# Optimization experiments

Measured on AMD Instinct MI355X. Metric: run time of the kernel, lower is better.

The kernel has to match this reference:

```python
import jax, jax.numpy as jnp
import numpy as np

N_CELLS, IN_DIM, HID, OUT = 65536, 128, 256, 128
MLP_H = 128   # engine MLP hidden width is hard-coded to 128 in the source
N_MORPH = 32  # min(32, n_cells//4)


def setup_inputs() -> dict:
    key = jax.random.key(0)
    ks = jax.random.split(key, 18)
    s = 0.05
    return {
        "x": jax.random.normal(ks[0], (1, IN_DIM), jnp.float32),
        "hiddens": jax.random.normal(ks[1], (N_CELLS, HID), jnp.float32) * 0.1,
        "Wa1": jax.random.normal(ks[2], (MLP_H, IN_DIM + HID), jnp.float32) * s,
        "ba1": jax.random.normal(ks[3], (MLP_H,), jnp.float32) * s,
        "Wa2": jax.random.normal(ks[4], (OUT, MLP_H), jnp.float32) * s,
        "ba2": jax.random.normal(ks[5], (OUT,), jnp.float32) * s,
        "Wg1": jax.random.normal(ks[6], (MLP_H, IN_DIM + HID), jnp.float32) * s,
        "bg1": jax.random.normal(ks[7], (MLP_H,), jnp.float32) * s,
        "Wg2": jax.random.normal(ks[8], (OUT, MLP_H), jnp.float32) * s,
        "bg2": jax.random.normal(ks[9], (OUT,), jnp.float32) * s,
        "W_ih": jax.random.normal(ks[10], (3 * HID, OUT + 1), jnp.float32) * s,
        "W_hh": jax.random.normal(ks[11], (3 * HID, HID), jnp.float32) * s,
        "b_ih": jax.random.normal(ks[12], (3 * HID,), jnp.float32) * s,
        "b_hh": jax.random.normal(ks[13], (3 * HID,), jnp.float32) * s,
        "nat_w": jnp.eye(HID, dtype=jnp.float32),  # nn.init.eye_
        "morph_w": jax.random.normal(ks[14], (N_MORPH, HID, HID), jnp.float32) * 0.02,
        "morph_src": jax.random.randint(ks[15], (N_MORPH,), 0, N_CELLS, jnp.int32),
        "morph_tgt": jax.random.randint(ks[16], (N_MORPH,), 0, N_CELLS, jnp.int32),
        "step": 0,
    }


def _forward(x, hiddens, Wa1, ba1, Wa2, ba2, Wg1, bg1, Wg2, bg2,
             W_ih, W_hh, b_ih, b_hh, nat_w, morph_w, morph_src, morph_tgt, step):
    n = hiddens.shape[0]
    # --- BenchMind, batched over all cells (x broadcast to every cell) ---
    xb = jnp.broadcast_to(x, (n, x.shape[-1]))
    combined = jnp.concatenate([xb, hiddens], axis=-1)               # [n, in+hid]
    a = jax.nn.relu(combined @ Wa1.T + ba1) @ Wa2.T + ba2            # [n, out]
    g = jax.nn.relu(combined @ Wg1.T + bg1) @ Wg2.T + bg2            # [n, out]
    out = a - g                                                       # [n, out]
    tension = jnp.mean(out * out, axis=-1, keepdims=True)            # [n, 1]
    # mem_input is detached in torch
    mem_in = jax.lax.stop_gradient(jnp.concatenate([out, tension], axis=-1))
    # --- PyTorch GRUCell math ---
    gi = mem_in @ W_ih.T + b_ih                                      # [n, 3H]
    gh = hiddens @ W_hh.T + b_hh                                     # [n, 3H]
    i_r, i_z, i_n = jnp.split(gi, 3, axis=-1)
    h_r, h_z, h_n = jnp.split(gh, 3, axis=-1)
    r = jax.nn.sigmoid(i_r + h_r)
    z = jax.nn.sigmoid(i_z + h_z)
    nn_ = jnp.tanh(i_n + r * h_n)
    hid = jax.lax.stop_gradient((1.0 - z) * nn_ + z * hiddens)       # detached new hiddens
    if step % 3 == 0:
        hid = jax.lax.stop_gradient(hid @ nat_w.T)                   # natural transformation
    # --- limit / colimit (morphism gather-transform-aggregate) ---
    limit = jnp.einsum('mij,mj->i', morph_w, hid[morph_src]) / N_MORPH
    colimit = jnp.einsum('mji,mj->i', morph_w, hid[morph_tgt]) / N_MORPH
    diff = limit - colimit
    cat_tension = jnp.mean(diff * diff)
    hid = hid + 0.05 * jax.lax.stop_gradient(diff)[None, :]
    # --- faction sync (+ debate if step > 5) ---
    n_f = min(8, n // 2)
    fs = n // n_f
    hf = hid[: n_f * fs].reshape(n_f, fs, hid.shape[-1])
    fmean = hf.mean(axis=1, keepdims=True)                           # [n_f,1,H]
    hf = 0.85 * hf + 0.15 * fmean
    if step > 5:
        global_op = hf.mean(axis=1).mean(axis=0)                     # mean of faction means
        dc = max(1, fs // 4)
        hf = hf.at[:, :dc].set(0.85 * hf[:, :dc] + 0.15 * global_op)
    hid = jnp.concatenate([hf.reshape(n_f * fs, -1), hid[n_f * fs:]], axis=0)
    # --- tension-weighted combination (weights detached: .item() in torch) ---
    t = jax.lax.stop_gradient(tension[:, 0])                         # [n]
    w = jax.nn.softmax(t, axis=0)
    combined_out = jnp.sum(w[:, None] * out, axis=0, keepdims=True)  # [1, out]
    avg_tension = jnp.mean(tension) + 0.1 * cat_tension
    return combined_out, avg_tension, hid


def reference(x, hiddens, Wa1, ba1, Wa2, ba2, Wg1, bg1, Wg2, bg2,
              W_ih, W_hh, b_ih, b_hh, nat_w, morph_w, morph_src, morph_tgt, step):
    combined_out, avg_tension, _ = _forward(
        x, hiddens, Wa1, ba1, Wa2, ba2, Wg1, bg1, Wg2, bg2,
        W_ih, W_hh, b_ih, b_hh, nat_w, morph_w, morph_src, morph_tgt, step)
    return combined_out, avg_tension
```

## Files before the change

kernel.cpp:

```cpp
#include <hip/hip_runtime.h>
#include <math.h>

#define OFF_W1B   0
#define OFF_W2A   32768
#define OFF_XW1B  49152
#define OFF_B2D   49408
#define OFF_PT    49536
#define OFF_PE    50560
#define OFF_POUT  51584
#define OFF_MI4   182656
#define OFF_TEN   190848
#define OFF_HH4   190912
#define OFF_GI    207296
#define OFF_GH    256448
#define OFF_PLIM  305600
#define OFF_PCOL8 313792
#define OFF_GMSK  379392

typedef short bf16x8 __attribute__((ext_vector_type(8)));
typedef short s16x4  __attribute__((ext_vector_type(4)));
typedef float f32x4  __attribute__((ext_vector_type(4)));

__device__ __forceinline__ unsigned short f2bf(float f) {
    unsigned u = __builtin_bit_cast(unsigned, f);
    u += 0x7FFFu + ((u >> 16) & 1u);
    return (unsigned short)(u >> 16);
}

__device__ __forceinline__ bf16x8 cvt8(float4 a, float4 b) {
    bf16x8 v;
    v[0] = (short)f2bf(a.x); v[1] = (short)f2bf(a.y);
    v[2] = (short)f2bf(a.z); v[3] = (short)f2bf(a.w);
    v[4] = (short)f2bf(b.x); v[5] = (short)f2bf(b.y);
    v[6] = (short)f2bf(b.z); v[7] = (short)f2bf(b.w);
    return v;
}

__global__ __launch_bounds__(256) void k_prep(
    const float* __restrict__ x, const float* __restrict__ hiddens,
    const float* __restrict__ Wa1, const float* __restrict__ ba1,
    const float* __restrict__ Wa2, const float* __restrict__ ba2,
    const float* __restrict__ Wg1, const float* __restrict__ bg1,
    const float* __restrict__ Wg2, const float* __restrict__ bg2,
    const int* __restrict__ msrc, const int* __restrict__ mtgt,
    float* __restrict__ ws)
{
    const int b = blockIdx.x, t = threadIdx.x;
    unsigned short* w1b = (unsigned short*)(ws + OFF_W1B);
    unsigned short* w2a = (unsigned short*)(ws + OFF_W2A);
    if (b < 256) {
        const int n = b;
        const float* row = (n < 128) ? &Wa1[n * 384] : &Wg1[(n - 128) * 384];
        const int kc = t >> 3;
        w1b[(kc * 256 + n) * 8 + (t & 7)] = f2bf(row[128 + t]);
        if (n < 128) {
            float w2 = (t < 128) ? Wa2[n * 128 + t] : -Wg2[n * 128 + (t - 128)];
            w2a[(kc * 128 + n) * 8 + (t & 7)] = f2bf(w2);
        }
    } else if (b == 256) {
        const int n = t;
        const float* wr = (n < 128) ? &Wa1[n * 384] : &Wg1[(n - 128) * 384];
        float s = (n < 128) ? ba1[n] : bg1[n - 128];
        for (int j = 0; j < 128; ++j) s = fmaf(x[j], wr[j], s);
        ws[OFF_XW1B + n] = s;
        if (n < 128) ws[OFF_B2D + n] = ba2[n] - bg2[n];
    } else if (b == 257) {
        unsigned long long* gm = (unsigned long long*)(ws + OFF_GMSK);
        for (int i = t; i < 1024; i += 256) gm[i] = 0ull;
        __syncthreads();
        if (t < 64) {
            const int cell = (t < 32) ? msrc[t] : mtgt[t - 32];
            atomicOr(&gm[cell >> 6], 1ull << t);
        }
    } else {
        const int g = b - 258;
        const int cell = (g < 32) ? msrc[g] : mtgt[g - 32];
        ws[OFF_HH4 + (t >> 2) * 256 + g * 4 + (t & 3)] = hiddens[(size_t)cell * 256 + t];
    }
}

__global__ __launch_bounds__(512, 2) void k_main(
    const float* __restrict__ hiddens,
    const int* __restrict__ msrc, const int* __restrict__ mtgt,
    float* __restrict__ ws)
{
    __shared__ __align__(16) short hB[64 * 256];
    __shared__ __align__(16) short h1B[64 * 256];
    __shared__ float part[512];
    __shared__ float e_sm[64], t_sm_[64];
    __shared__ int gid_sm[64];

    const int tid  = threadIdx.x;
    const int lane = tid & 63, wid = tid >> 6;
    const int l15 = lane & 15, l4 = lane >> 4;
    const int blk = blockIdx.x;

    if (tid < 64) gid_sm[tid] = (tid < 32) ? msrc[tid] : mtgt[tid - 32];

    const uint4* w1g = (const uint4*)(ws + OFF_W1B);
    const uint4* w2g = (const uint4*)(ws + OFF_W2A);
    const unsigned long long* gm = (const unsigned long long*)(ws + OFF_GMSK);

    const int rc = tid >> 3;
    const int q0 = (tid & 7) * 4;
    const float* hsrc = hiddens + (size_t)(blk * 128 + rc) * 256 + q0 * 8;

    float4 nx0, nx1, nx2, nx3, nx4, nx5, nx6, nx7;
    nx0 = *(const float4*)(hsrc + 0);  nx1 = *(const float4*)(hsrc + 4);
    nx2 = *(const float4*)(hsrc + 8);  nx3 = *(const float4*)(hsrc + 12);
    nx4 = *(const float4*)(hsrc + 16); nx5 = *(const float4*)(hsrc + 20);
    nx6 = *(const float4*)(hsrc + 24); nx7 = *(const float4*)(hsrc + 28);

    uint4 af[8][2], a2[8];
#pragma unroll
    for (int s = 0; s < 8; ++s) {
        af[s][0] = w1g[(s * 4 + l4) * 256 + wid * 32 + l15];
        af[s][1] = w1g[(s * 4 + l4) * 256 + wid * 32 + 16 + l15];
        a2[s]    = w2g[(s * 4 + l4) * 128 + wid * 16 + l15];
    }

    *(bf16x8*)&hB[rc * 256 + (((q0 + 0) ^ (rc & 15)) << 3)] = cvt8(nx0, nx1);
    *(bf16x8*)&hB[rc * 256 + (((q0 + 1) ^ (rc & 15)) << 3)] = cvt8(nx2, nx3);
    *(bf16x8*)&hB[rc * 256 + (((q0 + 2) ^ (rc & 15)) << 3)] = cvt8(nx4, nx5);
    *(bf16x8*)&hB[rc * 256 + (((q0 + 3) ^ (rc & 15)) << 3)] = cvt8(nx6, nx7);
    nx0 = *(const float4*)(hsrc + 16384 + 0);  nx1 = *(const float4*)(hsrc + 16384 + 4);
    nx2 = *(const float4*)(hsrc + 16384 + 8);  nx3 = *(const float4*)(hsrc + 16384 + 12);
    nx4 = *(const float4*)(hsrc + 16384 + 16); nx5 = *(const float4*)(hsrc + 16384 + 20);
    nx6 = *(const float4*)(hsrc + 16384 + 24); nx7 = *(const float4*)(hsrc + 16384 + 28);
    __syncthreads();

#pragma unroll
    for (int t = 0; t < 2; ++t) {
        const int bt = blk * 2 + t;

        f32x4 acc[2][4];
#pragma unroll
        for (int nf = 0; nf < 2; ++nf)
#pragma unroll
            for (int ct = 0; ct < 4; ++ct) acc[nf][ct] = (f32x4)0.f;

        __builtin_amdgcn_s_setprio(1);
#pragma unroll
        for (int s = 0; s < 8; ++s) {
            bf16x8 b[4];
#pragma unroll
            for (int ct = 0; ct < 4; ++ct) {
                const int c = ct * 16 + l15;
                b[ct] = *(const bf16x8*)&hB[c * 256 + (((s * 4 + l4) ^ (c & 15)) << 3)];
            }
#pragma unroll
            for (int nf = 0; nf < 2; ++nf) {
                const bf16x8 a = __builtin_bit_cast(bf16x8, af[s][nf]);
#pragma unroll
                for (int ct = 0; ct < 4; ++ct)
                    acc[nf][ct] = __builtin_amdgcn_mfma_f32_16x16x32_bf16(a, b[ct], acc[nf][ct], 0, 0, 0);
            }
        }
        __builtin_amdgcn_s_setprio(0);

#pragma unroll
        for (int nf = 0; nf < 2; ++nf) {
            const int n0 = wid * 32 + nf * 16 + l4 * 4;
            float4 xb = *(const float4*)(ws + OFF_XW1B + n0);
            const float bx[4] = {xb.x, xb.y, xb.z, xb.w};
            const int chunk = n0 >> 3;
            const int off = (l4 & 1) * 4;
#pragma unroll
            for (int ct = 0; ct < 4; ++ct) {
                const int c = ct * 16 + l15;
                s16x4 pk;
#pragma unroll
                for (int r = 0; r < 4; ++r)
                    pk[r] = (short)f2bf(fmaxf(acc[nf][ct][r] + bx[r], 0.f));
                *(s16x4*)&h1B[c * 256 + ((chunk ^ (c & 15)) << 3) + off] = pk;
            }
        }
        __syncthreads();

        f32x4 acc2[4];
#pragma unroll
        for (int ct = 0; ct < 4; ++ct) acc2[ct] = (f32x4)0.f;

        __builtin_amdgcn_s_setprio(1);
#pragma unroll
        for (int s = 0; s < 8; ++s) {
            bf16x8 b2[4];
#pragma unroll
            for (int ct = 0; ct < 4; ++ct) {
                const int c = ct * 16 + l15;
                b2[ct] = *(const bf16x8*)&h1B[c * 256 + (((s * 4 + l4) ^ (c & 15)) << 3)];
            }
            const bf16x8 a = __builtin_bit_cast(bf16x8, a2[s]);
#pragma unroll
            for (int ct = 0; ct < 4; ++ct)
                acc2[ct] = __builtin_amdgcn_mfma_f32_16x16x32_bf16(a, b2[ct], acc2[ct], 0, 0, 0);
        }
        __builtin_amdgcn_s_setprio(0);

        float outv[4][4];
        {
            float4 bd = *(const float4*)(ws + OFF_B2D + wid * 16 + l4 * 4);
            const float bv[4] = {bd.x, bd.y, bd.z, bd.w};
#pragma unroll
            for (int ct = 0; ct < 4; ++ct)
#pragma unroll
                for (int r = 0; r < 4; ++r)
                    outv[ct][r] = acc2[ct][r] + bv[r];
        }

#pragma unroll
        for (int ct = 0; ct < 4; ++ct) {
            float sq = 0.f;
#pragma unroll
            for (int r = 0; r < 4; ++r) sq = fmaf(outv[ct][r], outv[ct][r], sq);
            sq += __shfl_xor(sq, 16);
            sq += __shfl_xor(sq, 32);
            if (l4 == 0) part[wid * 64 + ct * 16 + l15] = sq;
        }
        __syncthreads();

        if (tid < 64) {
            float s = 0.f;
#pragma unroll
            for (int w = 0; w < 8; ++w) s += part[w * 64 + tid];
            const float tv = s * (1.f / 128.f);
            const float ev = expf(tv);
            t_sm_[tid] = tv; e_sm[tid] = ev;
            float pt = tv, pe = ev;
            for (int off = 32; off > 0; off >>= 1) {
                pt += __shfl_down(pt, off);
                pe += __shfl_down(pe, off);
            }
            if (tid == 0) { ws[OFF_PT + bt] = pt; ws[OFF_PE + bt] = pe; }
            unsigned long long m = gm[bt];
            while (m) {
                const int g = __builtin_ctzll(m); m &= m - 1;
                const int cg = gid_sm[g];
                if ((cg >> 6) == bt && (cg & 63) == tid) ws[OFF_TEN + g] = tv;
            }
        }
        __syncthreads();

        {
            float p[4];
#pragma unroll
            for (int r = 0; r < 4; ++r) {
                float s = 0.f;
#pragma unroll
                for (int ct = 0; ct < 4; ++ct)
                    s = fmaf(e_sm[ct * 16 + l15], outv[ct][r], s);
                p[r] = s;
            }
#pragma unroll
            for (int r = 0; r < 4; ++r) {
                p[r] += __shfl_xor(p[r], 1);
                p[r] += __shfl_xor(p[r], 2);
                p[r] += __shfl_xor(p[r], 4);
                p[r] += __shfl_xor(p[r], 8);
            }
            if (l15 == 0)
                *(float4*)(ws + OFF_POUT + (size_t)bt * 128 + wid * 16 + l4 * 4) =
                    make_float4(p[0], p[1], p[2], p[3]);
        }
        {
            unsigned long long m = gm[bt];
            while (m) {
                const int g = __builtin_ctzll(m); m &= m - 1;
                const int cg = gid_sm[g];
                if ((cg >> 6) != bt) continue;
                const int c = cg & 63;
                if ((c & 15) == l15) {
                    const int ct = c >> 4;
                    *(float4*)(ws + OFF_MI4 + (wid * 4 + l4) * 256 + g * 4) =
                        make_float4(outv[ct][0], outv[ct][1], outv[ct][2], outv[ct][3]);
                }
            }
        }

        if (t == 0) {
            *(bf16x8*)&hB[rc * 256 + (((q0 + 0) ^ (rc & 15)) << 3)] = cvt8(nx0, nx1);
            *(bf16x8*)&hB[rc * 256 + (((q0 + 1) ^ (rc & 15)) << 3)] = cvt8(nx2, nx3);
            *(bf16x8*)&hB[rc * 256 + (((q0 + 2) ^ (rc & 15)) << 3)] = cvt8(nx4, nx5);
            *(bf16x8*)&hB[rc * 256 + (((q0 + 3) ^ (rc & 15)) << 3)] = cvt8(nx6, nx7);
            __syncthreads();
        }
    }
}

__global__ __launch_bounds__(256) void k_tail1(
    const float* __restrict__ W_ih, const float* __restrict__ W_hh,
    const float* __restrict__ b_ih, const float* __restrict__ b_hh,
    float* __restrict__ ws)
{
    const int lane = threadIdx.x & 63;
    const int w    = threadIdx.x >> 6;
    const int row  = __builtin_amdgcn_readfirstlane(blockIdx.x * 4 + w);
    const float* mi4 = ws + OFF_MI4;
    const float* hh4 = ws + OFF_HH4;

    const float* wi = W_ih + row * 129;
    float gi = b_ih[row];
#pragma unroll 8
    for (int q = 0; q < 32; ++q) {
        float4 a = *(const float4*)(mi4 + q * 256 + lane * 4);
        gi = fmaf(wi[4 * q + 0], a.x, gi);
        gi = fmaf(wi[4 * q + 1], a.y, gi);
        gi = fmaf(wi[4 * q + 2], a.z, gi);
        gi = fmaf(wi[4 * q + 3], a.w, gi);
    }
    gi = fmaf(ws[OFF_TEN + lane], wi[128], gi);

    const float* wh = W_hh + (size_t)row * 256;
    float gh = b_hh[row];
#pragma unroll 8
    for (int q = 0; q < 64; ++q) {
        float4 a = *(const float4*)(hh4 + q * 256 + lane * 4);
        float4 b = *(const float4*)(wh + 4 * q);
        gh = fmaf(b.x, a.x, gh);
        gh = fmaf(b.y, a.y, gh);
        gh = fmaf(b.z, a.z, gh);
        gh = fmaf(b.w, a.w, gh);
    }
    ws[OFF_GI + lane * 768 + row] = gi;
    ws[OFF_GH + lane * 768 + row] = gh;
}

__global__ __launch_bounds__(256) void k_morph(
    const float* __restrict__ morph_w, const float* __restrict__ nat_w,
    const int* __restrict__ step, float* __restrict__ ws)
{
    __shared__ float wsm[32 * 264];
    __shared__ float hd0[256], hd1[256];
    __shared__ float hs[256], ht[256];
    const int blk = blockIdx.x, t = threadIdx.x;
    const int m = blk >> 3, ch = blk & 7;
    const float* wm = morph_w + (size_t)m * 65536 + (size_t)ch * 32 * 256;
    {
        const int r = t >> 3, c0 = (t & 7) * 32;
#pragma unroll
        for (int it = 0; it < 8; ++it)
            *(float4*)&wsm[r * 264 + c0 + it * 4] = *(const float4*)(wm + r * 256 + c0 + it * 4);
    }
#pragma unroll
    for (int h = 0; h < 2; ++h) {
        const int g = h * 32 + m;
        const float i_r = ws[OFF_GI + g * 768 + t];
        const float i_z = ws[OFF_GI + g * 768 + 256 + t];
        const float i_n = ws[OFF_GI + g * 768 + 512 + t];
        const float h_r = ws[OFF_GH + g * 768 + t];
        const float h_z = ws[OFF_GH + g * 768 + 256 + t];
        const float h_n = ws[OFF_GH + g * 768 + 512 + t];
        const float hv  = ws[OFF_HH4 + (t >> 2) * 256 + g * 4 + (t & 3)];
        const float r  = 1.f / (1.f + expf(-(i_r + h_r)));
        const float z  = 1.f / (1.f + expf(-(i_z + h_z)));
        const float nn = tanhf(i_n + r * h_n);
        const float hid = (1.f - z) * nn + z * hv;
        if (h == 0) hd0[t] = hid; else hd1[t] = hid;
    }
    __syncthreads();

    float hn0, hn1;
    if (step[0] % 3 == 0) {
        const float4* wr = (const float4*)(nat_w + (size_t)t * 256);
        float s0 = 0.f, s1 = 0.f;
        for (int q = 0; q < 64; ++q) {
            float4 wq = wr[q];
            s0 = fmaf(wq.x, hd0[4 * q + 0], s0); s1 = fmaf(wq.x, hd1[4 * q + 0], s1);
            s0 = fmaf(wq.y, hd0[4 * q + 1], s0); s1 = fmaf(wq.y, hd1[4 * q + 1], s1);
            s0 = fmaf(wq.z, hd0[4 * q + 2], s0); s1 = fmaf(wq.z, hd1[4 * q + 2], s1);
            s0 = fmaf(wq.w, hd0[4 * q + 3], s0); s1 = fmaf(wq.w, hd1[4 * q + 3], s1);
        }
        hn0 = s0; hn1 = s1;
    } else {
        hn0 = hd0[t]; hn1 = hd1[t];
    }
    hs[t] = hn0; ht[t] = hn1;
    __syncthreads();

    {
        const int il = t >> 3, jc = t & 7;
        float L = 0.f;
#pragma unroll 8
        for (int jj = 0; jj < 32; ++jj) {
            const int j = jc + 8 * jj;
            L = fmaf(wsm[il * 264 + j], hs[j], L);
        }
        L += __shfl_down(L, 4);
        L += __shfl_down(L, 2);
        L += __shfl_down(L, 1);
        if (jc == 0) ws[OFF_PLIM + m * 256 + ch * 32 + il] = L;
    }
    {
        float C = 0.f;
#pragma unroll 8
        for (int r = 0; r < 32; ++r)
            C = fmaf(wsm[r * 264 + t], ht[ch * 32 + r], C);
        ws[OFF_PCOL8 + blk * 256 + t] = C;
    }
}

__global__ __launch_bounds__(256) void k_out(const float* __restrict__ ws,
                                             float* __restrict__ out)
{
    __shared__ float red[256];
    const int b = blockIdx.x, t = threadIdx.x;
    if (b < 128) {
        float so = 0.f, se = 0.f;
        for (int i = t; i < 1024; i += 256) {
            so += ws[OFF_POUT + (size_t)i * 128 + b];
            se += ws[OFF_PE + i];
        }
        red[t] = so; __syncthreads();
        for (int s = 128; s > 0; s >>= 1) { if (t < s) red[t] += red[t + s]; __syncthreads(); }
        const float SO = red[0]; __syncthreads();
        red[t] = se; __syncthreads();
        for (int s = 128; s > 0; s >>= 1) { if (t < s) red[t] += red[t + s]; __syncthreads(); }
        if (t == 0) out[b] = SO / red[0];
    } else {
        float pt = 0.f;
        for (int i = t; i < 1024; i += 256) pt += ws[OFF_PT + i];
        float L = 0.f, C = 0.f;
        for (int m = 0; m < 32; ++m) L += ws[OFF_PLIM + m * 256 + t];
        for (int mc = 0; mc < 256; ++mc) C += ws[OFF_PCOL8 + mc * 256 + t];
        const float d = (L - C) * (1.f / 32.f);
        red[t] = d * d; __syncthreads();
        for (int s = 128; s > 0; s >>= 1) { if (t < s) red[t] += red[t + s]; __syncthreads(); }
        const float cat = red[0] * (1.f / 256.f); __syncthreads();
        red[t] = pt; __syncthreads();
        for (int s = 128; s > 0; s >>= 1) { if (t < s) red[t] += red[t + s]; __syncthreads(); }
        if (t == 0) out[128] = red[0] * (1.f / 65536.f) + 0.1f * cat;
    }
}

extern "C" void kernel_launch(void* const* d_in, const int* in_sizes, int n_in,
                              void* d_out, int out_size, void* d_ws, size_t ws_size,
                              hipStream_t stream)
{
    const float* x     = (const float*)d_in[0];
    const float* hidd  = (const float*)d_in[1];
    const float* Wa1   = (const float*)d_in[2];
    const float* ba1   = (const float*)d_in[3];
    const float* Wa2   = (const float*)d_in[4];
    const float* ba2   = (const float*)d_in[5];
    const float* Wg1   = (const float*)d_in[6];
    const float* bg1   = (const float*)d_in[7];
    const float* Wg2   = (const float*)d_in[8];
    const float* bg2   = (const float*)d_in[9];
    const float* W_ih  = (const float*)d_in[10];
    const float* W_hh  = (const float*)d_in[11];
    const float* b_ih  = (const float*)d_in[12];
    const float* b_hh  = (const float*)d_in[13];
    const float* nat_w = (const float*)d_in[14];
    const float* mw    = (const float*)d_in[15];
    const int*   msrc  = (const int*)d_in[16];
    const int*   mtgt  = (const int*)d_in[17];
    const int*   step  = (const int*)d_in[18];

    float* out = (float*)d_out;
    float* ws  = (float*)d_ws;

    k_prep <<<322, 256, 0, stream>>>(x, hidd, Wa1, ba1, Wa2, ba2, Wg1, bg1, Wg2, bg2, msrc, mtgt, ws);
    k_main <<<512, 512, 0, stream>>>(hidd, msrc, mtgt, ws);
    k_tail1<<<192, 256, 0, stream>>>(W_ih, W_hh, b_ih, b_hh, ws);
    k_morph<<<256, 256, 0, stream>>>(mw, nat_w, step, ws);
    k_out  <<<129, 256, 0, stream>>>(ws, out);
}
```

Before: 78.65 us.

## Switch main MLP kernel to 32x32 MFMA with 128-cell tiles and streamed weights

The main kernel now processes 128 cells per tile (256 per block, 256 blocks) and uses 32x32x16 bf16 MFMAs with a 2x2 wave tiling over hidden units and cells. Weight fragments are streamed from global memory with a two-step register prefetch instead of all being held in registers. The LDS tiles use padded rows with a 32-way XOR swizzle. Workspace offsets, the group-mask granularity and the reductions in k_out are adjusted for 512 tiles instead of 1024. The aim is more reuse per operand load and fewer blocks, at the cost of doubled LDS per block (which may limit occupancy) and weight reloads on every tile.

```diff
diff --git a/kernel.cpp b/kernel.cpp
--- a/kernel.cpp
+++ b/kernel.cpp
@@ -6,20 +6,22 @@
 #define OFF_XW1B  49152
 #define OFF_B2D   49408
 #define OFF_PT    49536
-#define OFF_PE    50560
-#define OFF_POUT  51584
-#define OFF_MI4   182656
-#define OFF_TEN   190848
-#define OFF_HH4   190912
-#define OFF_GI    207296
-#define OFF_GH    256448
-#define OFF_PLIM  305600
-#define OFF_PCOL8 313792
-#define OFF_GMSK  379392
+#define OFF_PE    50048
+#define OFF_POUT  50560
+#define OFF_MI4   181632
+#define OFF_TEN   189824
+#define OFF_HH4   189888
+#define OFF_GI    206272
+#define OFF_GH    255424
+#define OFF_PLIM  304576
+#define OFF_PCOL8 312768
+#define OFF_GMSK  378304
 
 typedef short bf16x8 __attribute__((ext_vector_type(8)));
 typedef short s16x4  __attribute__((ext_vector_type(4)));
-typedef float f32x4  __attribute__((ext_vector_type(4)));
+typedef float f32x16 __attribute__((ext_vector_type(16)));
+
+#define HS 272
 
 __device__ __forceinline__ unsigned short f2bf(float f) {
     unsigned u = __builtin_bit_cast(unsigned, f);
@@ -66,11 +68,11 @@
         if (n < 128) ws[OFF_B2D + n] = ba2[n] - bg2[n];
     } else if (b == 257) {
         unsigned long long* gm = (unsigned long long*)(ws + OFF_GMSK);
-        for (int i = t; i < 1024; i += 256) gm[i] = 0ull;
+        for (int i = t; i < 512; i += 256) gm[i] = 0ull;
         __syncthreads();
         if (t < 64) {
             const int cell = (t < 32) ? msrc[t] : mtgt[t - 32];
-            atomicOr(&gm[cell >> 6], 1ull << t);
+            atomicOr(&gm[cell >> 7], 1ull << t);
         }
     } else {
         const int g = b - 258;
@@ -84,15 +86,16 @@
     const int* __restrict__ msrc, const int* __restrict__ mtgt,
     float* __restrict__ ws)
 {
-    __shared__ __align__(16) short hB[64 * 256];
-    __shared__ __align__(16) short h1B[64 * 256];
+    __shared__ __align__(16) short hB[128 * HS];
+    __shared__ __align__(16) short h1B[128 * HS];
     __shared__ float part[512];
-    __shared__ float e_sm[64], t_sm_[64];
+    __shared__ float e_sm[128], t_sm_[128];
     __shared__ int gid_sm[64];
 
     const int tid  = threadIdx.x;
     const int lane = tid & 63, wid = tid >> 6;
-    const int l15 = lane & 15, l4 = lane >> 4;
+    const int l31 = lane & 31, h = lane >> 5;
+    const int wn = wid >> 1, wc = wid & 1;
     const int blk = blockIdx.x;
 
     if (tid < 64) gid_sm[tid] = (tid < 32) ? msrc[tid] : mtgt[tid - 32];
@@ -101,187 +104,191 @@
     const uint4* w2g = (const uint4*)(ws + OFF_W2A);
     const unsigned long long* gm = (const unsigned long long*)(ws + OFF_GMSK);
 
-    const int rc = tid >> 3;
-    const int q0 = (tid & 7) * 4;
-    const float* hsrc = hiddens + (size_t)(blk * 128 + rc) * 256 + q0 * 8;
-
-    float4 nx0, nx1, nx2, nx3, nx4, nx5, nx6, nx7;
-    nx0 = *(const float4*)(hsrc + 0);  nx1 = *(const float4*)(hsrc + 4);
-    nx2 = *(const float4*)(hsrc + 8);  nx3 = *(const float4*)(hsrc + 12);
-    nx4 = *(const float4*)(hsrc + 16); nx5 = *(const float4*)(hsrc + 20);
-    nx6 = *(const float4*)(hsrc + 24); nx7 = *(const float4*)(hsrc + 28);
-
-    uint4 af[8][2], a2[8];
-#pragma unroll
-    for (int s = 0; s < 8; ++s) {
-        af[s][0] = w1g[(s * 4 + l4) * 256 + wid * 32 + l15];
-        af[s][1] = w1g[(s * 4 + l4) * 256 + wid * 32 + 16 + l15];
-        a2[s]    = w2g[(s * 4 + l4) * 128 + wid * 16 + l15];
-    }
-
-    *(bf16x8*)&hB[rc * 256 + (((q0 + 0) ^ (rc & 15)) << 3)] = cvt8(nx0, nx1);
-    *(bf16x8*)&hB[rc * 256 + (((q0 + 1) ^ (rc & 15)) << 3)] = cvt8(nx2, nx3);
-    *(bf16x8*)&hB[rc * 256 + (((q0 + 2) ^ (rc & 15)) << 3)] = cvt8(nx4, nx5);
-    *(bf16x8*)&hB[rc * 256 + (((q0 + 3) ^ (rc & 15)) << 3)] = cvt8(nx6, nx7);
-    nx0 = *(const float4*)(hsrc + 16384 + 0);  nx1 = *(const float4*)(hsrc + 16384 + 4);
-    nx2 = *(const float4*)(hsrc + 16384 + 8);  nx3 = *(const float4*)(hsrc + 16384 + 12);
-    nx4 = *(const float4*)(hsrc + 16384 + 16); nx5 = *(const float4*)(hsrc + 16384 + 20);
-    nx6 = *(const float4*)(hsrc + 16384 + 24); nx7 = *(const float4*)(hsrc + 16384 + 28);
+    const int rc = tid >> 2;
+    const int kq = (tid & 3) * 8;
+    const float* hsrc = hiddens + (size_t)(blk * 256 + rc) * 256 + (tid & 3) * 64;
+
+    float4 nx[16];
+#pragma unroll
+    for (int i = 0; i < 16; ++i) nx[i] = *(const float4*)(hsrc + i * 4);
+#pragma unroll
+    for (int it = 0; it < 8; ++it) {
+        const int kc = kq + it;
+        *(bf16x8*)&hB[rc * HS + ((kc ^ (rc & 31)) << 3)] = cvt8(nx[2 * it], nx[2 * it + 1]);
+    }
+#pragma unroll
+    for (int i = 0; i < 16; ++i) nx[i] = *(const float4*)(hsrc + 128 * 256 + i * 4);
     __syncthreads();
+
+    const int c0 = wc * 64 + l31;
+    const int c1 = wc * 64 + 32 + l31;
 
 #pragma unroll
     for (int t = 0; t < 2; ++t) {
         const int bt = blk * 2 + t;
 
-        f32x4 acc[2][4];
-#pragma unroll
-        for (int nf = 0; nf < 2; ++nf)
-#pragma unroll
-            for (int ct = 0; ct < 4; ++ct) acc[nf][ct] = (f32x4)0.f;
+        f32x16 ac00 = (f32x16)0.f, ac01 = (f32x16)0.f;
+        f32x16 ac10 = (f32x16)0.f, ac11 = (f32x16)0.f;
+
+        uint4 a0c = w1g[(0 + h) * 256 + wn * 64 + l31];
+        uint4 a1c = w1g[(0 + h) * 256 + wn * 64 + 32 + l31];
+        uint4 a0n = w1g[(2 + h) * 256 + wn * 64 + l31];
+        uint4 a1n = w1g[(2 + h) * 256 + wn * 64 + 32 + l31];
+        uint4 g2a, g2b;
 
         __builtin_amdgcn_s_setprio(1);
 #pragma unroll
-        for (int s = 0; s < 8; ++s) {
-            bf16x8 b[4];
-#pragma unroll
-            for (int ct = 0; ct < 4; ++ct) {
-                const int c = ct * 16 + l15;
-                b[ct] = *(const bf16x8*)&hB[c * 256 + (((s * 4 + l4) ^ (c & 15)) << 3)];
-            }
-#pragma unroll
-            for (int nf = 0; nf < 2; ++nf) {
-                const bf16x8 a = __builtin_bit_cast(bf16x8, af[s][nf]);
-#pragma unroll
-                for (int ct = 0; ct < 4; ++ct)
-                    acc[nf][ct] = __builtin_amdgcn_mfma_f32_16x16x32_bf16(a, b[ct], acc[nf][ct], 0, 0, 0);
-            }
+        for (int s = 0; s < 16; ++s) {
+            uint4 a0f, a1f;
+            if (s < 14) {
+                a0f = w1g[((s + 2) * 2 + h) * 256 + wn * 64 + l31];
+                a1f = w1g[((s + 2) * 2 + h) * 256 + wn * 64 + 32 + l31];
+            } else if (s == 14) {
+                g2a = w2g[(0 + h) * 128 + wn * 32 + l31];
+            } else {
+                g2b = w2g[(2 + h) * 128 + wn * 32 + l31];
+            }
+            const int kc = s * 2 + h;
+            bf16x8 b0 = *(const bf16x8*)&hB[c0 * HS + ((kc ^ (c0 & 31)) << 3)];
+            bf16x8 b1 = *(const bf16x8*)&hB[c1 * HS + ((kc ^ (c1 & 31)) << 3)];
+            const bf16x8 A0 = __builtin_bit_cast(bf16x8, a0c);
+            const bf16x8 A1 = __builtin_bit_cast(bf16x8, a1c);
+            ac00 = __builtin_amdgcn_mfma_f32_32x32x16_bf16(A0, b0, ac00, 0, 0, 0);
+            ac01 = __builtin_amdgcn_mfma_f32_32x32x16_bf16(A0, b1, ac01, 0, 0, 0);
+            ac10 = __builtin_amdgcn_mfma_f32_32x32x16_bf16(A1, b0, ac10, 0, 0, 0);
+            ac11 = __builtin_amdgcn_mfma_f32_32x32x16_bf16(A1, b1, ac11, 0, 0, 0);
+            a0c = a0n; a1c = a1n;
+            if (s < 14) { a0n = a0f; a1n = a1f; }
         }
         __builtin_amdgcn_s_setprio(0);
 
 #pragma unroll
-        for (int nf = 0; nf < 2; ++nf) {
-            const int n0 = wid * 32 + nf * 16 + l4 * 4;
-            float4 xb = *(const float4*)(ws + OFF_XW1B + n0);
-            const float bx[4] = {xb.x, xb.y, xb.z, xb.w};
-            const int chunk = n0 >> 3;
-            const int off = (l4 & 1) * 4;
-#pragma unroll
-            for (int ct = 0; ct < 4; ++ct) {
-                const int c = ct * 16 + l15;
-                s16x4 pk;
-#pragma unroll
-                for (int r = 0; r < 4; ++r)
-                    pk[r] = (short)f2bf(fmaxf(acc[nf][ct][r] + bx[r], 0.f));
-                *(s16x4*)&h1B[c * 256 + ((chunk ^ (c & 15)) << 3) + off] = pk;
+        for (int nt = 0; nt < 2; ++nt) {
+#pragma unroll
+            for (int rr = 0; rr < 4; ++rr) {
+                const int nb = wn * 64 + nt * 32 + rr * 8 + 4 * h;
+                float4 xb = *(const float4*)(ws + OFF_XW1B + nb);
+                const float bx[4] = {xb.x, xb.y, xb.z, xb.w};
+                const int chunk = nb >> 3;
+                const f32x16& aa0 = nt ? ac10 : ac00;
+                const f32x16& aa1 = nt ? ac11 : ac01;
+                s16x4 p0, p1;
+#pragma unroll
+                for (int q = 0; q < 4; ++q) {
+                    p0[q] = (short)f2bf(fmaxf(aa0[rr * 4 + q] + bx[q], 0.f));
+                    p1[q] = (short)f2bf(fmaxf(aa1[rr * 4 + q] + bx[q], 0.f));
+                }
+                *(s16x4*)&h1B[c0 * HS + ((chunk ^ (c0 & 31)) << 3) + 4 * h] = p0;
+                *(s16x4*)&h1B[c1 * HS + ((chunk ^ (c1 & 31)) << 3) + 4 * h] = p1;
             }
         }
         __syncthreads();
 
-        f32x4 acc2[4];
-#pragma unroll
-        for (int ct = 0; ct < 4; ++ct) acc2[ct] = (f32x4)0.f;
-
+        f32x16 d0 = (f32x16)0.f, d1 = (f32x16)0.f;
         __builtin_amdgcn_s_setprio(1);
 #pragma unroll
-        for (int s = 0; s < 8; ++s) {
-            bf16x8 b2[4];
-#pragma unroll
-            for (int ct = 0; ct < 4; ++ct) {
-                const int c = ct * 16 + l15;
-                b2[ct] = *(const bf16x8*)&h1B[c * 256 + (((s * 4 + l4) ^ (c & 15)) << 3)];
-            }
-            const bf16x8 a = __builtin_bit_cast(bf16x8, a2[s]);
-#pragma unroll
-            for (int ct = 0; ct < 4; ++ct)
-                acc2[ct] = __builtin_amdgcn_mfma_f32_16x16x32_bf16(a, b2[ct], acc2[ct], 0, 0, 0);
+        for (int s = 0; s < 16; ++s) {
+            uint4 gf;
+            if (s < 14) gf = w2g[((s + 2) * 2 + h) * 128 + wn * 32 + l31];
+            const int kc = s * 2 + h;
+            bf16x8 b0 = *(const bf16x8*)&h1B[c0 * HS + ((kc ^ (c0 & 31)) << 3)];
+            bf16x8 b1 = *(const bf16x8*)&h1B[c1 * HS + ((kc ^ (c1 & 31)) << 3)];
+            const bf16x8 A = __builtin_bit_cast(bf16x8, g2a);
+            d0 = __builtin_amdgcn_mfma_f32_32x32x16_bf16(A, b0, d0, 0, 0, 0);
+            d1 = __builtin_amdgcn_mfma_f32_32x32x16_bf16(A, b1, d1, 0, 0, 0);
+            g2a = g2b;
+            if (s < 14) g2b = gf;
         }
         __builtin_amdgcn_s_setprio(0);
 
-        float outv[4][4];
-        {
-            float4 bd = *(const float4*)(ws + OFF_B2D + wid * 16 + l4 * 4);
+        float outv[2][16];
+#pragma unroll
+        for (int rr = 0; rr < 4; ++rr) {
+            float4 bd = *(const float4*)(ws + OFF_B2D + wn * 32 + rr * 8 + 4 * h);
             const float bv[4] = {bd.x, bd.y, bd.z, bd.w};
 #pragma unroll
-            for (int ct = 0; ct < 4; ++ct)
-#pragma unroll
-                for (int r = 0; r < 4; ++r)
-                    outv[ct][r] = acc2[ct][r] + bv[r];
-        }
-
-#pragma unroll
-        for (int ct = 0; ct < 4; ++ct) {
+            for (int q = 0; q < 4; ++q) {
+                outv[0][rr * 4 + q] = d0[rr * 4 + q] + bv[q];
+                outv[1][rr * 4 + q] = d1[rr * 4 + q] + bv[q];
+            }
+        }
+
+#pragma unroll
+        for (int ct = 0; ct < 2; ++ct) {
             float sq = 0.f;
 #pragma unroll
-            for (int r = 0; r < 4; ++r) sq = fmaf(outv[ct][r], outv[ct][r], sq);
-            sq += __shfl_xor(sq, 16);
+            for (int r = 0; r < 16; ++r) sq = fmaf(outv[ct][r], outv[ct][r], sq);
             sq += __shfl_xor(sq, 32);
-            if (l4 == 0) part[wid * 64 + ct * 16 + l15] = sq;
+            if (h == 0) part[wn * 128 + wc * 64 + ct * 32 + l31] = sq;
         }
         __syncthreads();
 
-        if (tid < 64) {
-            float s = 0.f;
-#pragma unroll
-            for (int w = 0; w < 8; ++w) s += part[w * 64 + tid];
-            const float tv = s * (1.f / 128.f);
+        if (tid < 128) {
+            const float tv = (part[tid] + part[128 + tid] + part[256 + tid] + part[384 + tid]) * (1.f / 128.f);
             const float ev = expf(tv);
             t_sm_[tid] = tv; e_sm[tid] = ev;
-            float pt = tv, pe = ev;
-            for (int off = 32; off > 0; off >>= 1) {
-                pt += __shfl_down(pt, off);
-                pe += __shfl_down(pe, off);
-            }
-            if (tid == 0) { ws[OFF_PT + bt] = pt; ws[OFF_PE + bt] = pe; }
             unsigned long long m = gm[bt];
             while (m) {
                 const int g = __builtin_ctzll(m); m &= m - 1;
                 const int cg = gid_sm[g];
-                if ((cg >> 6) == bt && (cg & 63) == tid) ws[OFF_TEN + g] = tv;
+                if ((cg >> 7) == bt && (cg & 127) == tid) ws[OFF_TEN + g] = tv;
             }
         }
         __syncthreads();
 
+        if (tid < 64) {
+            float pt = t_sm_[tid] + t_sm_[64 + tid];
+            float pe = e_sm[tid] + e_sm[64 + tid];
+            for (int off = 32; off > 0; off >>= 1) {
+                pt += __shfl_down(pt, off);
+                pe += __shfl_down(pe, off);
+            }
+            if (tid == 0) { ws[OFF_PT + bt] = pt; ws[OFF_PE + bt] = pe; }
+        }
+
         {
-            float p[4];
-#pragma unroll
-            for (int r = 0; r < 4; ++r) {
-                float s = 0.f;
-#pragma unroll
-                for (int ct = 0; ct < 4; ++ct)
-                    s = fmaf(e_sm[ct * 16 + l15], outv[ct][r], s);
-                p[r] = s;
-            }
-#pragma unroll
-            for (int r = 0; r < 4; ++r) {
-                p[r] += __shfl_xor(p[r], 1);
-                p[r] += __shfl_xor(p[r], 2);
-                p[r] += __shfl_xor(p[r], 4);
-                p[r] += __shfl_xor(p[r], 8);
-            }
-            if (l15 == 0)
-                *(float4*)(ws + OFF_POUT + (size_t)bt * 128 + wid * 16 + l4 * 4) =
-                    make_float4(p[0], p[1], p[2], p[3]);
+            const float e0 = e_sm[wc * 64 + l31], e1 = e_sm[wc * 64 + 32 + l31];
+#pragma unroll
+            for (int rr = 0; rr < 4; ++rr)
+#pragma unroll
+                for (int q = 0; q < 4; ++q) {
+                    const int r = rr * 4 + q;
+                    float s = fmaf(e0, outv[0][r], e1 * outv[1][r]);
+                    s += __shfl_xor(s, 1);
+                    s += __shfl_xor(s, 2);
+                    s += __shfl_xor(s, 4);
+                    s += __shfl_xor(s, 8);
+                    s += __shfl_xor(s, 16);
+                    if (l31 == 0)
+                        ws[OFF_POUT + (size_t)(bt * 2 + wc) * 128 + wn * 32 + rr * 8 + 4 * h + q] = s;
+                }
         }
         {
             unsigned long long m = gm[bt];
             while (m) {
                 const int g = __builtin_ctzll(m); m &= m - 1;
                 const int cg = gid_sm[g];
-                if ((cg >> 6) != bt) continue;
-                const int c = cg & 63;
-                if ((c & 15) == l15) {
-                    const int ct = c >> 4;
-                    *(float4*)(ws + OFF_MI4 + (wid * 4 + l4) * 256 + g * 4) =
-                        make_float4(outv[ct][0], outv[ct][1], outv[ct][2], outv[ct][3]);
+                if ((cg >> 7) != bt) continue;
+                const int cp = cg & 127;
+                if ((cp >> 6) == wc && (cp & 31) == l31) {
+                    const int ct = (cp >> 5) & 1;
+#pragma unroll
+                    for (int rr = 0; rr < 4; ++rr)
+#pragma unroll
+                        for (int q = 0; q < 4; ++q) {
+                            const int qq = 8 * wn + 2 * rr + h;
+                            ws[OFF_MI4 + qq * 256 + g * 4 + q] = outv[ct][rr * 4 + q];
+                        }
                 }
             }
         }
 
         if (t == 0) {
-            *(bf16x8*)&hB[rc * 256 + (((q0 + 0) ^ (rc & 15)) << 3)] = cvt8(nx0, nx1);
-            *(bf16x8*)&hB[rc * 256 + (((q0 + 1) ^ (rc & 15)) << 3)] = cvt8(nx2, nx3);
-            *(bf16x8*)&hB[rc * 256 + (((q0 + 2) ^ (rc & 15)) << 3)] = cvt8(nx4, nx5);
-            *(bf16x8*)&hB[rc * 256 + (((q0 + 3) ^ (rc & 15)) << 3)] = cvt8(nx6, nx7);
+#pragma unroll
+            for (int it = 0; it < 8; ++it) {
+                const int kc = kq + it;
+                *(bf16x8*)&hB[rc * HS + ((kc ^ (rc & 31)) << 3)] = cvt8(nx[2 * it], nx[2 * it + 1]);
+            }
             __syncthreads();
         }
     }
@@ -342,8 +349,8 @@
             *(float4*)&wsm[r * 264 + c0 + it * 4] = *(const float4*)(wm + r * 256 + c0 + it * 4);
     }
 #pragma unroll
-    for (int h = 0; h < 2; ++h) {
-        const int g = h * 32 + m;
+    for (int hh = 0; hh < 2; ++hh) {
+        const int g = hh * 32 + m;
         const float i_r = ws[OFF_GI + g * 768 + t];
         const float i_z = ws[OFF_GI + g * 768 + 256 + t];
         const float i_n = ws[OFF_GI + g * 768 + 512 + t];
@@ -355,7 +362,7 @@
         const float z  = 1.f / (1.f + expf(-(i_z + h_z)));
         const float nn = tanhf(i_n + r * h_n);
         const float hid = (1.f - z) * nn + z * hv;
-        if (h == 0) hd0[t] = hid; else hd1[t] = hid;
+        if (hh == 0) hd0[t] = hid; else hd1[t] = hid;
     }
     __syncthreads();
 
@@ -406,10 +413,8 @@
     const int b = blockIdx.x, t = threadIdx.x;
     if (b < 128) {
         float so = 0.f, se = 0.f;
-        for (int i = t; i < 1024; i += 256) {
-            so += ws[OFF_POUT + (size_t)i * 128 + b];
-            se += ws[OFF_PE + i];
-        }
+        for (int i = t; i < 1024; i += 256) so += ws[OFF_POUT + (size_t)i * 128 + b];
+        for (int i = t; i < 512; i += 256) se += ws[OFF_PE + i];
         red[t] = so; __syncthreads();
         for (int s = 128; s > 0; s >>= 1) { if (t < s) red[t] += red[t + s]; __syncthreads(); }
         const float SO = red[0]; __syncthreads();
@@ -418,7 +423,7 @@
         if (t == 0) out[b] = SO / red[0];
     } else {
         float pt = 0.f;
-        for (int i = t; i < 1024; i += 256) pt += ws[OFF_PT + i];
+        for (int i = t; i < 512; i += 256) pt += ws[OFF_PT + i];
         float L = 0.f, C = 0.f;
         for (int m = 0; m < 32; ++m) L += ws[OFF_PLIM + m * 256 + t];
         for (int mc = 0; mc < 256; ++mc) C += ws[OFF_PCOL8 + mc * 256 + t];
@@ -460,7 +465,7 @@
     float* ws  = (float*)d_ws;
 
     k_prep <<<322, 256, 0, stream>>>(x, hidd, Wa1, ba1, Wa2, ba2, Wg1, bg1, Wg2, bg2, msrc, mtgt, ws);
-    k_main <<<512, 512, 0, stream>>>(hidd, msrc, mtgt, ws);
+    k_main <<<256, 512, 0, stream>>>(hidd, msrc, mtgt, ws);
     k_tail1<<<192, 256, 0, stream>>>(W_ih, W_hh, b_ih, b_hh, ws);
     k_morph<<<256, 256, 0, stream>>>(mw, nat_w, step, ws);
     k_out  <<<129, 256, 0, stream>>>(ws, out);
```

Result: slower. 96.52 us (+22.7%).
